# Kernel tuning notes

Hardware: AMD Instinct MI355X
Metric: run time of the kernel (lower is better)

Reference implementation:

```python
import jax, jax.numpy as jnp
import numpy as np

N = 131072   # octree nodes at this depth
C = 192      # channels (depthwise)
K = 27       # 3x3x3 neighbor stencil
BN_EPS = 1e-5


def setup_inputs() -> dict:
    key = jax.random.key(0)
    k1, k2, k3 = jax.random.split(key, 3)
    data = jax.random.normal(k1, (N, C), dtype=jnp.float32)
    # Octree neighbor table: for each node, indices of its 27 stencil neighbors.
    neigh = jax.random.randint(k2, (N, K), 0, N)
    # Depthwise weights [K, C] (OctreeDWConv, use_bias=False)
    weight = jax.random.normal(k3, (K, C), dtype=jnp.float32) * 0.05
    gamma = jnp.ones((C,), dtype=jnp.float32)
    beta = jnp.zeros((C,), dtype=jnp.float32)
    return {"data": data, "neigh": neigh, "weight": weight,
            "gamma": gamma, "beta": beta}


def reference(data, neigh, weight, gamma, beta):
    # Depthwise octree conv: out[n, c] = sum_k data[neigh[n, k], c] * weight[k, c]
    # Scan over the 27 stencil taps so we never materialize the [N, K, C] gather.
    def step(acc, kin):
        idx_k, w_k = kin          # idx_k: [N], w_k: [C]
        return acc + data[idx_k] * w_k, None

    acc0 = jnp.zeros_like(data)
    out, _ = jax.lax.scan(step, acc0, (neigh.T, weight))  # out: [N, C]

    # BatchNorm1d (training mode: batch statistics over the node dimension)
    mean = jnp.mean(out, axis=0)
    var = jnp.var(out, axis=0)
    return (out - mean) * jax.lax.rsqrt(var + BN_EPS) * gamma + beta
```

## Files before the change

kernel.cpp:

```cpp
#include <hip/hip_runtime.h>


static constexpr int NN = 131072;
static constexpr int CC = 192;
static constexpr int KK = 27;
static constexpr int NB = 32;
static constexpr float BN_EPS = 1e-5f;

__device__ __forceinline__ unsigned short f2bf_rne(float x) {
    unsigned u = __float_as_uint(x);
    return (unsigned short)((u + 0x7FFFu + ((u >> 16) & 1u)) >> 16);
}

__global__ __launch_bounds__(256) void cvt_bf16(
    const float* __restrict__ src,
    unsigned short* __restrict__ dst)
{
    const int i = blockIdx.x * 256 + threadIdx.x;
    const float4 v = reinterpret_cast<const float4*>(src)[i];
    ushort4 o;
    o.x = f2bf_rne(v.x);
    o.y = f2bf_rne(v.y);
    o.z = f2bf_rne(v.z);
    o.w = f2bf_rne(v.w);
    reinterpret_cast<ushort4*>(dst)[i] = o;
}

__global__ __launch_bounds__(CC) void conv_bn_partial_bf16(
    const unsigned short* __restrict__ data_bf,
    const int*   __restrict__ neigh,
    const float* __restrict__ weight,
    float*       __restrict__ conv_out,
    float*       __restrict__ ch_sum,
    float*       __restrict__ ch_sumsq)
{
    const int c    = threadIdx.x;
    const int base = blockIdx.x * NB;

    float w[KK];
#pragma unroll
    for (int k = 0; k < KK; ++k) w[k] = weight[k * CC + c];

    float s = 0.f, ss = 0.f;

    for (int n = 0; n < NB; ++n) {
        const int node = base + n;
        const int* nrow = neigh + node * KK;
        float acc = 0.f;
#pragma unroll
        for (int k = 0; k < KK; ++k) {
            const int idx = nrow[k];
            const float v = __uint_as_float(
                (unsigned)data_bf[idx * CC + c] << 16);
            acc = fmaf(v, w[k], acc);
        }
        conv_out[node * CC + c] = acc;
        s  += acc;
        ss += acc * acc;
    }

    atomicAdd(&ch_sum[c],   s);
    atomicAdd(&ch_sumsq[c], ss);
}

__global__ __launch_bounds__(CC) void conv_bn_partial_f32(
    const float* __restrict__ data,
    const int*   __restrict__ neigh,
    const float* __restrict__ weight,
    float*       __restrict__ conv_out,
    float*       __restrict__ ch_sum,
    float*       __restrict__ ch_sumsq)
{
    const int c    = threadIdx.x;
    const int base = blockIdx.x * NB;

    float w[KK];
#pragma unroll
    for (int k = 0; k < KK; ++k) w[k] = weight[k * CC + c];

    float s = 0.f, ss = 0.f;

    for (int n = 0; n < NB; ++n) {
        const int node = base + n;
        const int* nrow = neigh + node * KK;
        float acc = 0.f;
#pragma unroll
        for (int k = 0; k < KK; ++k) {
            acc = fmaf(data[nrow[k] * CC + c], w[k], acc);
        }
        conv_out[node * CC + c] = acc;
        s  += acc;
        ss += acc * acc;
    }

    atomicAdd(&ch_sum[c],   s);
    atomicAdd(&ch_sumsq[c], ss);
}

__global__ __launch_bounds__(CC) void bn_finalize(
    const float* __restrict__ ch_sum,
    const float* __restrict__ ch_sumsq,
    const float* __restrict__ gamma,
    const float* __restrict__ beta,
    float*       __restrict__ scale,
    float*       __restrict__ bias)
{
    const int c = threadIdx.x;
    const float inv_n = 1.0f / (float)NN;
    const float m  = ch_sum[c] * inv_n;
    const float v  = ch_sumsq[c] * inv_n - m * m;
    const float sc = gamma[c] * rsqrtf(v + BN_EPS);
    scale[c] = sc;
    bias[c]  = beta[c] - m * sc;
}

__global__ __launch_bounds__(256) void bn_apply(
    float* __restrict__ out,
    const float* __restrict__ scale,
    const float* __restrict__ bias)
{
    const int i = blockIdx.x * 256 + threadIdx.x;
    const int cb = (i % (CC / 4)) * 4;

    float4 v  = reinterpret_cast<float4*>(out)[i];
    const float4 sc = *reinterpret_cast<const float4*>(scale + cb);
    const float4 bi = *reinterpret_cast<const float4*>(bias + cb);
    v.x = fmaf(v.x, sc.x, bi.x);
    v.y = fmaf(v.y, sc.y, bi.y);
    v.z = fmaf(v.z, sc.z, bi.z);
    v.w = fmaf(v.w, sc.w, bi.w);
    reinterpret_cast<float4*>(out)[i] = v;
}

extern "C" void kernel_launch(void* const* d_in, const int* in_sizes, int n_in,
                              void* d_out, int out_size, void* d_ws, size_t ws_size,
                              hipStream_t stream) {
    const float* data   = (const float*)d_in[0];
    const int*   neigh  = (const int*)  d_in[1];
    const float* weight = (const float*)d_in[2];
    const float* gamma  = (const float*)d_in[3];
    const float* beta   = (const float*)d_in[4];
    float* out = (float*)d_out;

    float* ch_sum   = (float*)d_ws;
    float* ch_sumsq = ch_sum + CC;
    float* scale    = ch_sumsq + CC;
    float* bias     = scale + CC;
    unsigned short* data_bf =
        (unsigned short*)((char*)d_ws + 4096);
    const size_t need = 4096 + (size_t)NN * CC * sizeof(unsigned short);

    hipMemsetAsync(ch_sum, 0, 2 * CC * sizeof(float), stream);

    if (ws_size >= need) {
        cvt_bf16<<<(NN * CC / 4) / 256, 256, 0, stream>>>(data, data_bf);
        conv_bn_partial_bf16<<<NN / NB, CC, 0, stream>>>(
            data_bf, neigh, weight, out, ch_sum, ch_sumsq);
    } else {
        conv_bn_partial_f32<<<NN / NB, CC, 0, stream>>>(
            data, neigh, weight, out, ch_sum, ch_sumsq);
    }
    bn_finalize<<<1, CC, 0, stream>>>(ch_sum, ch_sumsq, gamma, beta, scale, bias);
    bn_apply<<<(NN * CC / 4) / 256, 256, 0, stream>>>(out, scale, bias);
}
```

Baseline: 421.0 us.

## Vectorize bf16 gather 4 channels per thread and stage conv output in bf16

The conv kernel now has each thread handle 4 channels over 4 nodes at a time, with 8-byte gathers of bf16 data. Neighbor indices and weights are staged in LDS, and per-channel stats are reduced in LDS before the global atomics. When workspace allows, the intermediate conv result is written as bf16 and expanded in a new bn_apply kernel, which cuts intermediate write and read traffic. The risk is extra rounding of the pre-normalization values to bf16, and the BN statistics are still computed from the unrounded fp32 values.

```diff
diff --git a/kernel.cpp b/kernel.cpp
--- a/kernel.cpp
+++ b/kernel.cpp
@@ -11,56 +11,87 @@
     unsigned u = __float_as_uint(x);
     return (unsigned short)((u + 0x7FFFu + ((u >> 16) & 1u)) >> 16);
 }
+__device__ __forceinline__ unsigned pack2bf(float a, float b) {
+    return (unsigned)f2bf_rne(a) | ((unsigned)f2bf_rne(b) << 16);
+}
 
 __global__ __launch_bounds__(256) void cvt_bf16(
-    const float* __restrict__ src,
-    unsigned short* __restrict__ dst)
+    const float* __restrict__ src, unsigned short* __restrict__ dst)
 {
     const int i = blockIdx.x * 256 + threadIdx.x;
     const float4 v = reinterpret_cast<const float4*>(src)[i];
     ushort4 o;
-    o.x = f2bf_rne(v.x);
-    o.y = f2bf_rne(v.y);
-    o.z = f2bf_rne(v.z);
-    o.w = f2bf_rne(v.w);
+    o.x = f2bf_rne(v.x); o.y = f2bf_rne(v.y);
+    o.z = f2bf_rne(v.z); o.w = f2bf_rne(v.w);
     reinterpret_cast<ushort4*>(dst)[i] = o;
 }
 
-__global__ __launch_bounds__(CC) void conv_bn_partial_bf16(
+template<bool BF_OUT>
+__global__ __launch_bounds__(192) void conv4(
     const unsigned short* __restrict__ data_bf,
     const int*   __restrict__ neigh,
     const float* __restrict__ weight,
-    float*       __restrict__ conv_out,
+    float*       __restrict__ out_f32,
+    uint2*       __restrict__ out_bf,
     float*       __restrict__ ch_sum,
     float*       __restrict__ ch_sumsq)
 {
-    const int c    = threadIdx.x;
+    __shared__ __align__(16) float lds_w[KK * CC];
+    __shared__ int   lds_idx[NB * KK];
+    __shared__ float lds_s[CC];
+    __shared__ float lds_q[CC];
+
+    const int t = threadIdx.x;
+    const int g = t / 48;
+    const int q = t - g * 48;
     const int base = blockIdx.x * NB;
 
-    float w[KK];
-#pragma unroll
-    for (int k = 0; k < KK; ++k) w[k] = weight[k * CC + c];
-
-    float s = 0.f, ss = 0.f;
-
-    for (int n = 0; n < NB; ++n) {
-        const int node = base + n;
-        const int* nrow = neigh + node * KK;
-        float acc = 0.f;
+#pragma unroll
+    for (int k = 0; k < KK; ++k) lds_w[k * CC + t] = weight[k * CC + t];
+    for (int i = t; i < NB * KK; i += 192) lds_idx[i] = neigh[base * KK + i];
+    lds_s[t] = 0.f; lds_q[t] = 0.f;
+    __syncthreads();
+
+    const unsigned short* dptr = data_bf + q * 4;
+
+    float s0 = 0, s1 = 0, s2 = 0, s3 = 0;
+    float q0 = 0, q1 = 0, q2 = 0, q3 = 0;
+
+    for (int sstep = 0; sstep < NB / 4; ++sstep) {
+        const int ln = sstep * 4 + g;
+        float a0 = 0, a1 = 0, a2 = 0, a3 = 0;
 #pragma unroll
         for (int k = 0; k < KK; ++k) {
-            const int idx = nrow[k];
-            const float v = __uint_as_float(
-                (unsigned)data_bf[idx * CC + c] << 16);
-            acc = fmaf(v, w[k], acc);
+            const int idx = lds_idx[ln * KK + k];
+            const uint2 u = *reinterpret_cast<const uint2*>(
+                dptr + (size_t)idx * CC);
+            const float4 w4 = *reinterpret_cast<const float4*>(
+                &lds_w[k * CC + q * 4]);
+            a0 = fmaf(__uint_as_float(u.x << 16),         w4.x, a0);
+            a1 = fmaf(__uint_as_float(u.x & 0xFFFF0000u), w4.y, a1);
+            a2 = fmaf(__uint_as_float(u.y << 16),         w4.z, a2);
+            a3 = fmaf(__uint_as_float(u.y & 0xFFFF0000u), w4.w, a3);
         }
-        conv_out[node * CC + c] = acc;
-        s  += acc;
-        ss += acc * acc;
+        const int node = base + ln;
+        if (BF_OUT) {
+            uint2 o; o.x = pack2bf(a0, a1); o.y = pack2bf(a2, a3);
+            out_bf[node * 48 + q] = o;
+        } else {
+            float4 o = make_float4(a0, a1, a2, a3);
+            reinterpret_cast<float4*>(out_f32)[node * 48 + q] = o;
+        }
+        s0 += a0; s1 += a1; s2 += a2; s3 += a3;
+        q0 += a0 * a0; q1 += a1 * a1; q2 += a2 * a2; q3 += a3 * a3;
     }
 
-    atomicAdd(&ch_sum[c],   s);
-    atomicAdd(&ch_sumsq[c], ss);
+    const int cb = q * 4;
+    atomicAdd(&lds_s[cb + 0], s0); atomicAdd(&lds_s[cb + 1], s1);
+    atomicAdd(&lds_s[cb + 2], s2); atomicAdd(&lds_s[cb + 3], s3);
+    atomicAdd(&lds_q[cb + 0], q0); atomicAdd(&lds_q[cb + 1], q1);
+    atomicAdd(&lds_q[cb + 2], q2); atomicAdd(&lds_q[cb + 3], q3);
+    __syncthreads();
+    atomicAdd(&ch_sum[t],   lds_s[t]);
+    atomicAdd(&ch_sumsq[t], lds_q[t]);
 }
 
 __global__ __launch_bounds__(CC) void conv_bn_partial_f32(
@@ -71,39 +102,30 @@
     float*       __restrict__ ch_sum,
     float*       __restrict__ ch_sumsq)
 {
-    const int c    = threadIdx.x;
+    const int c = threadIdx.x;
     const int base = blockIdx.x * NB;
-
     float w[KK];
 #pragma unroll
     for (int k = 0; k < KK; ++k) w[k] = weight[k * CC + c];
-
     float s = 0.f, ss = 0.f;
-
     for (int n = 0; n < NB; ++n) {
         const int node = base + n;
         const int* nrow = neigh + node * KK;
         float acc = 0.f;
 #pragma unroll
-        for (int k = 0; k < KK; ++k) {
+        for (int k = 0; k < KK; ++k)
             acc = fmaf(data[nrow[k] * CC + c], w[k], acc);
-        }
         conv_out[node * CC + c] = acc;
-        s  += acc;
-        ss += acc * acc;
+        s += acc; ss += acc * acc;
     }
-
-    atomicAdd(&ch_sum[c],   s);
+    atomicAdd(&ch_sum[c], s);
     atomicAdd(&ch_sumsq[c], ss);
 }
 
 __global__ __launch_bounds__(CC) void bn_finalize(
-    const float* __restrict__ ch_sum,
-    const float* __restrict__ ch_sumsq,
-    const float* __restrict__ gamma,
-    const float* __restrict__ beta,
-    float*       __restrict__ scale,
-    float*       __restrict__ bias)
+    const float* __restrict__ ch_sum, const float* __restrict__ ch_sumsq,
+    const float* __restrict__ gamma,  const float* __restrict__ beta,
+    float* __restrict__ scale, float* __restrict__ bias)
 {
     const int c = threadIdx.x;
     const float inv_n = 1.0f / (float)NN;
@@ -114,21 +136,35 @@
     bias[c]  = beta[c] - m * sc;
 }
 
+__global__ __launch_bounds__(256) void bn_apply_bf16(
+    const uint2* __restrict__ conv_bf,
+    const float* __restrict__ scale, const float* __restrict__ bias,
+    float* __restrict__ out)
+{
+    const int i = blockIdx.x * 256 + threadIdx.x;
+    const int cb = (i % 48) * 4;
+    const uint2 u = conv_bf[i];
+    const float4 sc = *reinterpret_cast<const float4*>(scale + cb);
+    const float4 bi = *reinterpret_cast<const float4*>(bias + cb);
+    float4 v;
+    v.x = fmaf(__uint_as_float(u.x << 16),         sc.x, bi.x);
+    v.y = fmaf(__uint_as_float(u.x & 0xFFFF0000u), sc.y, bi.y);
+    v.z = fmaf(__uint_as_float(u.y << 16),         sc.z, bi.z);
+    v.w = fmaf(__uint_as_float(u.y & 0xFFFF0000u), sc.w, bi.w);
+    reinterpret_cast<float4*>(out)[i] = v;
+}
+
 __global__ __launch_bounds__(256) void bn_apply(
     float* __restrict__ out,
-    const float* __restrict__ scale,
-    const float* __restrict__ bias)
+    const float* __restrict__ scale, const float* __restrict__ bias)
 {
     const int i = blockIdx.x * 256 + threadIdx.x;
-    const int cb = (i % (CC / 4)) * 4;
-
-    float4 v  = reinterpret_cast<float4*>(out)[i];
+    const int cb = (i % 48) * 4;
+    float4 v = reinterpret_cast<float4*>(out)[i];
     const float4 sc = *reinterpret_cast<const float4*>(scale + cb);
     const float4 bi = *reinterpret_cast<const float4*>(bias + cb);
-    v.x = fmaf(v.x, sc.x, bi.x);
-    v.y = fmaf(v.y, sc.y, bi.y);
-    v.z = fmaf(v.z, sc.z, bi.z);
-    v.w = fmaf(v.w, sc.w, bi.w);
+    v.x = fmaf(v.x, sc.x, bi.x); v.y = fmaf(v.y, sc.y, bi.y);
+    v.z = fmaf(v.z, sc.z, bi.z); v.w = fmaf(v.w, sc.w, bi.w);
     reinterpret_cast<float4*>(out)[i] = v;
 }
 
@@ -146,20 +182,36 @@
     float* ch_sumsq = ch_sum + CC;
     float* scale    = ch_sumsq + CC;
     float* bias     = scale + CC;
-    unsigned short* data_bf =
-        (unsigned short*)((char*)d_ws + 4096);
-    const size_t need = 4096 + (size_t)NN * CC * sizeof(unsigned short);
+    unsigned short* data_bf = (unsigned short*)((char*)d_ws + 4096);
+    const size_t stage_bytes = (size_t)NN * CC * sizeof(unsigned short);
+    uint2* conv_bf = (uint2*)((char*)d_ws + 4096 + stage_bytes);
+
+    const size_t need_data = 4096 + stage_bytes;
+    const size_t need_full = 4096 + 2 * stage_bytes;
 
     hipMemsetAsync(ch_sum, 0, 2 * CC * sizeof(float), stream);
 
-    if (ws_size >= need) {
-        cvt_bf16<<<(NN * CC / 4) / 256, 256, 0, stream>>>(data, data_bf);
-        conv_bn_partial_bf16<<<NN / NB, CC, 0, stream>>>(
-            data_bf, neigh, weight, out, ch_sum, ch_sumsq);
+    const int vec_grid = (NN * CC / 4) / 256;
+
+    if (ws_size >= need_full) {
+        cvt_bf16<<<vec_grid, 256, 0, stream>>>(data, data_bf);
+        conv4<true><<<NN / NB, 192, 0, stream>>>(
+            data_bf, neigh, weight, nullptr, conv_bf, ch_sum, ch_sumsq);
+        bn_finalize<<<1, CC, 0, stream>>>(ch_sum, ch_sumsq, gamma, beta,
+                                          scale, bias);
+        bn_apply_bf16<<<vec_grid, 256, 0, stream>>>(conv_bf, scale, bias, out);
+    } else if (ws_size >= need_data) {
+        cvt_bf16<<<vec_grid, 256, 0, stream>>>(data, data_bf);
+        conv4<false><<<NN / NB, 192, 0, stream>>>(
+            data_bf, neigh, weight, out, nullptr, ch_sum, ch_sumsq);
+        bn_finalize<<<1, CC, 0, stream>>>(ch_sum, ch_sumsq, gamma, beta,
+                                          scale, bias);
+        bn_apply<<<vec_grid, 256, 0, stream>>>(out, scale, bias);
     } else {
         conv_bn_partial_f32<<<NN / NB, CC, 0, stream>>>(
             data, neigh, weight, out, ch_sum, ch_sumsq);
+        bn_finalize<<<1, CC, 0, stream>>>(ch_sum, ch_sumsq, gamma, beta,
+                                          scale, bias);
+        bn_apply<<<vec_grid, 256, 0, stream>>>(out, scale, bias);
     }
-    bn_finalize<<<1, CC, 0, stream>>>(ch_sum, ch_sumsq, gamma, beta, scale, bias);
-    bn_apply<<<(NN * CC / 4) / 256, 256, 0, stream>>>(out, scale, bias);
-}
+}
```

Measured after the change: 535.1 us. +27.1%, slower.
